# Kernel optimization log

Measured on AMD Instinct MI355X. Metric: run time of the kernel, lower is better.

Reference implementation:

```python
import jax, jax.numpy as jnp
import numpy as np
from jax import lax

RATIO = 0.5          # SAModule ratio
RADIUS = 0.15        # SAModule r
MAX_NBR = 64         # max_num_neighbors hardcoded in forward
F_IN, H1, H2, F_OUT = 64 + 3, 64, 64, 128  # local_nn MLP dims (x_j || pos_j - pos_i)


def _mlp(h, W1, b1, W2, b2, W3, b3):
    h = jax.nn.relu(h @ W1 + b1)
    h = jax.nn.relu(h @ W2 + b2)
    return jax.nn.relu(h @ W3 + b3)


def _fps_cloud(pos_c, m):
    # Farthest point sampling on one cloud [N,3]; deterministic start at index 0.
    n = pos_c.shape[0]
    def step(carry, _):
        mind, last = carry
        d = jnp.sum((pos_c - pos_c[last]) ** 2, axis=-1)
        mind = jnp.minimum(mind, d)
        nxt = jnp.argmax(mind).astype(jnp.int32)
        return (mind, nxt), last
    init = (jnp.full((n,), jnp.inf, pos_c.dtype), jnp.int32(0))
    _, sel = lax.scan(step, init, None, length=m)
    return sel  # [m] int32


def setup_inputs() -> dict:
    key = jax.random.key(0)
    ks = jax.random.split(key, 8)
    B, N, F = 8, 4096, 64
    x = jax.random.normal(ks[0], (B * N, F), jnp.float32)
    pos = jax.random.uniform(ks[1], (B * N, 3), jnp.float32)
    batch = jnp.repeat(jnp.arange(B, dtype=jnp.int64), N)
    s1 = 1.0 / np.sqrt(F_IN); s2 = 1.0 / np.sqrt(H1); s3 = 1.0 / np.sqrt(H2)
    W1 = jax.random.normal(ks[2], (F_IN, H1), jnp.float32) * s1
    b1 = jnp.zeros((H1,), jnp.float32)
    W2 = jax.random.normal(ks[3], (H1, H2), jnp.float32) * s2
    b2 = jnp.zeros((H2,), jnp.float32)
    W3 = jax.random.normal(ks[4], (H2, F_OUT), jnp.float32) * s3
    b3 = jnp.zeros((F_OUT,), jnp.float32)
    return {"x": x, "pos": pos, "batch": batch,
            "W1": W1, "b1": b1, "W2": W2, "b2": b2, "W3": W3, "b3": b3}


def reference(x, pos, batch, W1, b1, W2, b2, W3, b3):
    B = int(batch[-1]) + 1
    N = x.shape[0] // B
    M = int(N * RATIO)
    F = x.shape[1]
    xb = x.reshape(B, N, F)
    pb = pos.reshape(B, N, 3)

    # 1) fps(pos, batch, ratio)
    sel = jax.vmap(lambda p: _fps_cloud(p, M))(pb)                 # [B, M]
    q = jnp.take_along_axis(pb, sel[:, :, None], axis=1)           # [B, M, 3] centroid positions

    # 2) radius(pos, pos[idx], r, max_num_neighbors=64): keep the 64 nearest within r
    d2 = jnp.sum((q[:, :, None, :] - pb[:, None, :, :]) ** 2, -1)  # [B, M, N]
    score = jnp.where(d2 <= RADIUS ** 2, -d2, -jnp.inf)
    vals, nbr = lax.top_k(score, MAX_NBR)                          # [B, M, K]
    valid = vals > -jnp.inf                                        # centroid itself is always valid

    # 3) PointNetConv: message = net([x_j, pos_j - pos_i]); aggr = max
    xj = jax.vmap(lambda xc, i: xc[i])(xb, nbr)                    # [B, M, K, F]
    pj = jax.vmap(lambda pc, i: pc[i])(pb, nbr)                    # [B, M, K, 3]
    feat = jnp.concatenate([xj, pj - q[:, :, None, :]], axis=-1)   # [B, M, K, F+3]
    h = _mlp(feat, W1, b1, W2, b2, W3, b3)                         # [B, M, K, F_OUT]
    h = jnp.where(valid[..., None], h, -jnp.inf)
    out = jnp.max(h, axis=2)                                       # [B, M, F_OUT]

    x_out = out.reshape(B * M, -1)
    pos_out = q.reshape(B * M, 3)
    batch_out = jnp.repeat(jnp.arange(B, dtype=batch.dtype), M)
    return x_out, pos_out, batch_out
```

## Files before the change

### kernel.cpp

```cpp
#include <hip/hip_runtime.h>

typedef unsigned short u16;
typedef unsigned int u32;
typedef unsigned long long u64;

#define NB 8
#define NPTS 4096
#define MSEL 2048
#define NCENT (NB*MSEL)
#define KNBR 64
#define FEAT 64
#define FIN 67
#define HH 64
#define FOUT 128
#define CAND_CAP 192

#define KP1 96
#define SA 104
#define S2 72

typedef __attribute__((ext_vector_type(8))) short short8;
typedef __attribute__((ext_vector_type(4))) float f32x4;

__device__ __forceinline__ float bf2f(u16 u) {
    union { u32 i; float f; } v; v.i = ((u32)u) << 16; return v.f;
}
__device__ __forceinline__ u16 f2bf(float f) {
    union { float f; u32 i; } v; v.f = f;
    u32 x = v.i;
    x += 0x7fffu + ((x >> 16) & 1u);
    return (u16)(x >> 16);
}
__device__ __forceinline__ void splitbf(float a, u16& hi, u16& lo) {
    u16 h = f2bf(a);
    hi = h;
    lo = f2bf(__fsub_rn(a, bf2f(h)));
}

__device__ __forceinline__ int wave_max_i(int v) {
    int u;
    u = __builtin_amdgcn_update_dpp(v, v, 0x111, 0xf, 0xf, false); v = max(v, u);
    u = __builtin_amdgcn_update_dpp(v, v, 0x112, 0xf, 0xf, false); v = max(v, u);
    u = __builtin_amdgcn_update_dpp(v, v, 0x114, 0xf, 0xf, false); v = max(v, u);
    u = __builtin_amdgcn_update_dpp(v, v, 0x118, 0xf, 0xf, false); v = max(v, u);
    u = __builtin_amdgcn_update_dpp(v, v, 0x142, 0xf, 0xf, false); v = max(v, u);
    u = __builtin_amdgcn_update_dpp(v, v, 0x143, 0xf, 0xf, false); v = max(v, u);
    return __builtin_amdgcn_readlane(v, 63);
}
__device__ __forceinline__ int wave_min_i(int v) {
    int u;
    u = __builtin_amdgcn_update_dpp(v, v, 0x111, 0xf, 0xf, false); v = min(v, u);
    u = __builtin_amdgcn_update_dpp(v, v, 0x112, 0xf, 0xf, false); v = min(v, u);
    u = __builtin_amdgcn_update_dpp(v, v, 0x114, 0xf, 0xf, false); v = min(v, u);
    u = __builtin_amdgcn_update_dpp(v, v, 0x118, 0xf, 0xf, false); v = min(v, u);
    u = __builtin_amdgcn_update_dpp(v, v, 0x142, 0xf, 0xf, false); v = min(v, u);
    u = __builtin_amdgcn_update_dpp(v, v, 0x143, 0xf, 0xf, false); v = min(v, u);
    return __builtin_amdgcn_readlane(v, 63);
}

__global__ __launch_bounds__(256) void fps_kernel(const float* __restrict__ pos,
        int* __restrict__ sel, float* __restrict__ pos_out,
        float* __restrict__ batch_out) {
    __shared__ float px[NPTS], py[NPTS], pz[NPTS];
    __shared__ int hist[MSEL];
    __shared__ int4  sA[2][4];
    __shared__ float sZ[2][4];
    const int b = blockIdx.x, t = threadIdx.x;
    const int wid = t >> 6;
    const float* pb = pos + (long)b * NPTS * 3;

    for (int i = t; i < NPTS; i += 256) {
        px[i] = pb[i*3+0]; py[i] = pb[i*3+1]; pz[i] = pb[i*3+2];
    }
    __syncthreads();

    float rx[16], ry[16], rz[16], md[16];
    #pragma unroll
    for (int j = 0; j < 16; ++j) {
        int i = t + 256*j;
        rx[j] = px[i]; ry[j] = py[i]; rz[j] = pz[i];
        md[j] = __builtin_inff();
    }

    int cur = 0;
    float cx = px[0], cy = py[0], cz = pz[0];
    for (int s = 0; s < MSEL; ++s) {
        const int p = s & 1;
        if (t == 0) hist[s] = cur;
        float bv = -1.0f; int bi = 0;
        #pragma unroll
        for (int j = 0; j < 16; ++j) {
            float dx = __fsub_rn(rx[j], cx);
            float dy = __fsub_rn(ry[j], cy);
            float dz = __fsub_rn(rz[j], cz);
            float d  = __fadd_rn(__fadd_rn(__fmul_rn(dx,dx), __fmul_rn(dy,dy)),
                                 __fmul_rn(dz,dz));
            float m = fminf(md[j], d);
            md[j] = m;
            if (m > bv) { bv = m; bi = t + 256*j; }
        }
        const int fb = (int)__float_as_uint(bv);
        const int Mw = wave_max_i(fb);
        const int cnd = (fb == Mw) ? bi : 0x7fffffff;
        const int Iw = wave_min_i(cnd);
        if (t == (Iw & 255)) {
            int j = Iw >> 8;
            sA[p][wid] = make_int4(Mw, Iw, __float_as_int(rx[j]),
                                   __float_as_int(ry[j]));
            sZ[p][wid] = rz[j];
        }
        __syncthreads();
        int4 v0 = sA[p][0];
        int M = v0.x, I = v0.y;
        float nx = __int_as_float(v0.z), ny = __int_as_float(v0.w), nz = sZ[p][0];
        #pragma unroll
        for (int w = 1; w < 4; ++w) {
            int4 vw = sA[p][w];
            if (vw.x > M || (vw.x == M && vw.y < I)) {
                M = vw.x; I = vw.y;
                nx = __int_as_float(vw.z); ny = __int_as_float(vw.w);
                nz = sZ[p][w];
            }
        }
        cur = I; cx = nx; cy = ny; cz = nz;
    }
    __syncthreads();
    for (int g = t; g < MSEL; g += 256) {
        int i = hist[g];
        int o = b * MSEL + g;
        sel[o] = i;
        pos_out[o*3+0] = px[i]; pos_out[o*3+1] = py[i]; pos_out[o*3+2] = pz[i];
        batch_out[o] = (float)b;
    }
}

__global__ __launch_bounds__(256) void wcvt_kernel(const float* __restrict__ W1,
        const float* __restrict__ W2, const float* __restrict__ W3,
        u16* __restrict__ w1h, u16* __restrict__ w1l,
        u16* __restrict__ w2h, u16* __restrict__ w2l,
        u16* __restrict__ w3h, u16* __restrict__ w3l) {
    int t = blockIdx.x * 256 + threadIdx.x;
    if (t < 64*KP1) {
        int n = t / KP1, k = t % KP1;
        u16 h, l; splitbf((k < FIN) ? W1[(long)k*HH + n] : 0.0f, h, l);
        w1h[t] = h; w1l[t] = l;
    }
    if (t < 64*64) {
        int n = t / 64, k = t % 64;
        u16 h, l; splitbf(W2[(long)k*HH + n], h, l);
        w2h[t] = h; w2l[t] = l;
    }
    if (t < 128*64) {
        int n = t / 64, k = t % 64;
        u16 h, l; splitbf(W3[(long)k*FOUT + n], h, l);
        w3h[t] = h; w3l[t] = l;
    }
}

__global__ __launch_bounds__(256) void conv_kernel(const float* __restrict__ x,
        const float* __restrict__ pos, const int* __restrict__ sel,
        const u16* __restrict__ w1h, const u16* __restrict__ w1l,
        const u16* __restrict__ w2h, const u16* __restrict__ w2l,
        const u16* __restrict__ w3h, const u16* __restrict__ w3l,
        const float* __restrict__ b1, const float* __restrict__ b2,
        const float* __restrict__ b3, float* __restrict__ xout) {
    __shared__ __align__(16) u16 fAh[64*SA], fAl[64*SA];
    __shared__ __align__(16) u16 h1h[64*S2], h1l[64*S2];
    __shared__ float cdv[CAND_CAP];
    __shared__ int   cixv[CAND_CAP];
    __shared__ int   snbr[KNBR];
    __shared__ int   sc[2];
    const int c = blockIdx.x, t = threadIdx.x;
    const int b = c >> 11;
    const int lane = t & 63, w = t >> 6;
    const int colc = lane & 15;
    const float* pb = pos + (long)b * NPTS * 3;
    const int j0 = sel[c];
    const float qx = pb[j0*3+0], qy = pb[j0*3+1], qz = pb[j0*3+2];

    const int nw = w*16 + colc;
    const float bias1 = b1[nw];
    const float bias2 = b2[nw];
    const float bias3[2] = { b3[(2*w+0)*16 + colc], b3[(2*w+1)*16 + colc] };

    if (t == 0) { sc[0] = 0; sc[1] = 0; }
    __syncthreads();

    const float R2 = (float)(0.15 * 0.15);
    for (int it = 0; it < NPTS/256; ++it) {
        int i = t + 256*it;
        float dx = __fsub_rn(qx, pb[i*3+0]);
        float dy = __fsub_rn(qy, pb[i*3+1]);
        float dz = __fsub_rn(qz, pb[i*3+2]);
        float d2 = __fadd_rn(__fadd_rn(__fmul_rn(dx,dx), __fmul_rn(dy,dy)),
                             __fmul_rn(dz,dz));
        if (d2 <= R2) {
            int slot = atomicAdd(&sc[0], 1);
            if (slot < CAND_CAP) { cdv[slot] = d2; cixv[slot] = i; }
        }
    }
    __syncthreads();
    int C = sc[0]; if (C > CAND_CAP) C = CAND_CAP;
    int cnt;
    if (C <= KNBR) {
        for (int e = t; e < C; e += 256) snbr[e] = cixv[e];
        cnt = C;
    } else {
        for (int e = t; e < C; e += 256) {
            float de = cdv[e]; int ie = cixv[e];
            int rank = 0;
            for (int f = 0; f < C; ++f) {
                float df = cdv[f]; int jf = cixv[f];
                rank += (df < de || (df == de && jf < ie)) ? 1 : 0;
            }
            if (rank < KNBR) {
                int slot = atomicAdd(&sc[1], 1);
                snbr[slot] = ie;
            }
        }
        cnt = KNBR;
    }
    __syncthreads();

    const int kk = t >> 2, sub = t & 3;
    if (kk < cnt) {
        int j = snbr[kk];
        const float4* xr4 = (const float4*)(x + ((long)b*NPTS + j) * FEAT);
        #pragma unroll
        for (int i = 0; i < 4; ++i) {
            int ci = sub*4 + i;
            float4 v = xr4[ci];
            u16 h0,l0,h1_,l1_,h2_,l2_,h3_,l3_;
            splitbf(v.x, h0, l0); splitbf(v.y, h1_, l1_);
            splitbf(v.z, h2_, l2_); splitbf(v.w, h3_, l3_);
            int o = kk*SA + ci*4;
            fAh[o+0]=h0; fAh[o+1]=h1_; fAh[o+2]=h2_; fAh[o+3]=h3_;
            fAl[o+0]=l0; fAl[o+1]=l1_; fAl[o+2]=l2_; fAl[o+3]=l3_;
        }
        if (sub < 3) {
            float qv = (sub == 0) ? qx : ((sub == 1) ? qy : qz);
            u16 h, l; splitbf(__fsub_rn(pb[j*3+sub], qv), h, l);
            fAh[kk*SA + 64 + sub] = h; fAl[kk*SA + 64 + sub] = l;
        } else {
            fAh[kk*SA + 67] = 0; fAl[kk*SA + 67] = 0;
        }
        u32* zh = (u32*)&fAh[kk*SA + 68];
        u32* zl = (u32*)&fAl[kk*SA + 68];
        #pragma unroll
        for (int i2 = 0; i2 < 4; ++i2) { zh[sub + 4*i2] = 0; zl[sub + 4*i2] = 0; }
    }
    __syncthreads();

    const int mL = lane & 15;
    const int kq = (lane >> 4) * 8;
    const int rgrp = (lane >> 4) * 4;

    short8 B1h[3], B1l[3], B2h[2], B2l[2], B3h[2][2], B3l[2][2];
    #pragma unroll
    for (int i = 0; i < 3; ++i) {
        B1h[i] = *(const short8*)&w1h[nw*KP1 + i*32 + kq];
        B1l[i] = *(const short8*)&w1l[nw*KP1 + i*32 + kq];
    }
    #pragma unroll
    for (int i = 0; i < 2; ++i) {
        B2h[i] = *(const short8*)&w2h[nw*64 + i*32 + kq];
        B2l[i] = *(const short8*)&w2l[nw*64 + i*32 + kq];
    }

    #pragma unroll
    for (int rt = 0; rt < 4; ++rt) {
        short8 ah[3], al[3];
        #pragma unroll
        for (int i = 0; i < 3; ++i) {
            ah[i] = *(const short8*)&fAh[(rt*16 + mL)*SA + i*32 + kq];
            al[i] = *(const short8*)&fAl[(rt*16 + mL)*SA + i*32 + kq];
        }
        f32x4 acc = {bias1, bias1, bias1, bias1};
        #pragma unroll
        for (int i = 0; i < 3; ++i)
            acc = __builtin_amdgcn_mfma_f32_16x16x32_bf16(ah[i], B1h[i], acc, 0,0,0);
        #pragma unroll
        for (int i = 0; i < 3; ++i)
            acc = __builtin_amdgcn_mfma_f32_16x16x32_bf16(ah[i], B1l[i], acc, 0,0,0);
        #pragma unroll
        for (int i = 0; i < 3; ++i)
            acc = __builtin_amdgcn_mfma_f32_16x16x32_bf16(al[i], B1h[i], acc, 0,0,0);
        #pragma unroll
        for (int r = 0; r < 4; ++r) {
            u16 h, l; splitbf(fmaxf(acc[r], 0.0f), h, l);
            int mr = rt*16 + rgrp + r;
            h1h[mr*S2 + nw] = h; h1l[mr*S2 + nw] = l;
        }
    }
    #pragma unroll
    for (int j = 0; j < 2; ++j) {
        int n3 = (2*w + j)*16 + colc;
        #pragma unroll
        for (int i = 0; i < 2; ++i) {
            B3h[j][i] = *(const short8*)&w3h[n3*64 + i*32 + kq];
            B3l[j][i] = *(const short8*)&w3l[n3*64 + i*32 + kq];
        }
    }
    __syncthreads();

    #pragma unroll
    for (int rt = 0; rt < 4; ++rt) {
        short8 ah[2], al[2];
        #pragma unroll
        for (int i = 0; i < 2; ++i) {
            ah[i] = *(const short8*)&h1h[(rt*16 + mL)*S2 + i*32 + kq];
            al[i] = *(const short8*)&h1l[(rt*16 + mL)*S2 + i*32 + kq];
        }
        f32x4 acc = {bias2, bias2, bias2, bias2};
        #pragma unroll
        for (int i = 0; i < 2; ++i)
            acc = __builtin_amdgcn_mfma_f32_16x16x32_bf16(ah[i], B2h[i], acc, 0,0,0);
        #pragma unroll
        for (int i = 0; i < 2; ++i)
            acc = __builtin_amdgcn_mfma_f32_16x16x32_bf16(ah[i], B2l[i], acc, 0,0,0);
        #pragma unroll
        for (int i = 0; i < 2; ++i)
            acc = __builtin_amdgcn_mfma_f32_16x16x32_bf16(al[i], B2h[i], acc, 0,0,0);
        #pragma unroll
        for (int r = 0; r < 4; ++r) {
            u16 h, l; splitbf(fmaxf(acc[r], 0.0f), h, l);
            int mr = rt*16 + rgrp + r;
            fAh[mr*S2 + nw] = h; fAl[mr*S2 + nw] = l;
        }
    }
    __syncthreads();

    #pragma unroll
    for (int j = 0; j < 2; ++j) {
        const float bb = bias3[j];
        float v = 0.0f;
        #pragma unroll
        for (int rt = 0; rt < 4; ++rt) {
            short8 ah[2], al[2];
            #pragma unroll
            for (int i = 0; i < 2; ++i) {
                ah[i] = *(const short8*)&fAh[(rt*16 + mL)*S2 + i*32 + kq];
                al[i] = *(const short8*)&fAl[(rt*16 + mL)*S2 + i*32 + kq];
            }
            f32x4 acc = {bb, bb, bb, bb};
            #pragma unroll
            for (int i = 0; i < 2; ++i)
                acc = __builtin_amdgcn_mfma_f32_16x16x32_bf16(ah[i], B3h[j][i], acc, 0,0,0);
            #pragma unroll
            for (int i = 0; i < 2; ++i)
                acc = __builtin_amdgcn_mfma_f32_16x16x32_bf16(ah[i], B3l[j][i], acc, 0,0,0);
            #pragma unroll
            for (int i = 0; i < 2; ++i)
                acc = __builtin_amdgcn_mfma_f32_16x16x32_bf16(al[i], B3h[j][i], acc, 0,0,0);
            #pragma unroll
            for (int r = 0; r < 4; ++r) {
                int m = rt*16 + rgrp + r;
                float hv = fmaxf(acc[r], 0.0f);
                v = (m < cnt) ? fmaxf(v, hv) : v;
            }
        }
        v = fmaxf(v, __shfl_xor(v, 16, 64));
        v = fmaxf(v, __shfl_xor(v, 32, 64));
        if (lane < 16)
            xout[(long)c*FOUT + (2*w + j)*16 + lane] = v;
    }
}

extern "C" void kernel_launch(void* const* d_in, const int* in_sizes, int n_in,
                              void* d_out, int out_size, void* d_ws, size_t ws_size,
                              hipStream_t stream) {
    const float* x   = (const float*)d_in[0];
    const float* pos = (const float*)d_in[1];
    const float* W1 = (const float*)d_in[3];
    const float* b1 = (const float*)d_in[4];
    const float* W2 = (const float*)d_in[5];
    const float* b2 = (const float*)d_in[6];
    const float* W3 = (const float*)d_in[7];
    const float* b3 = (const float*)d_in[8];

    float* out       = (float*)d_out;
    float* xout      = out;
    float* pos_out   = out + (long)NCENT * FOUT;
    float* batch_out = pos_out + (long)NCENT * 3;

    int* sel = (int*)d_ws;
    u16* w1h = (u16*)((char*)d_ws + 65536);
    u16* w1l = w1h + 64*KP1;
    u16* w2h = w1l + 64*KP1;
    u16* w2l = w2h + 64*64;
    u16* w3h = w2l + 64*64;
    u16* w3l = w3h + 128*64;

    wcvt_kernel<<<32, 256, 0, stream>>>(W1, W2, W3, w1h, w1l, w2h, w2l, w3h, w3l);
    fps_kernel<<<NB, 256, 0, stream>>>(pos, sel, pos_out, batch_out);
    conv_kernel<<<NCENT, 256, 0, stream>>>(x, pos, sel, w1h, w1l, w2h, w2l,
                                           w3h, w3l, b1, b2, b3, xout);
}
```

Before: 1.950 ms.

## Widen FPS block to 512 threads with packed 64-bit DPP argmax reduction

The farthest-point-sampling kernel now runs 512 threads per cloud, so each thread holds 8 points instead of 16. The per-thread argmax becomes a tree over the 8 registers. The wave reduction packs distance and inverted index into one 64-bit key, replacing the separate max and min DPP passes. The cross-wave merge of 8 candidates also uses DPP across lanes rather than a serial loop in every thread. The aim is to shorten the 2048-step serial critical path of FPS, at the cost of more waves in the per-step barrier and more DPP traffic per step.

```diff
diff --git a/kernel.cpp b/kernel.cpp
--- a/kernel.cpp
+++ b/kernel.cpp
@@ -19,6 +19,8 @@
 #define SA 104
 #define S2 72
 
+#define FPT 512
+
 typedef __attribute__((ext_vector_type(8))) short short8;
 typedef __attribute__((ext_vector_type(4))) float f32x4;
 
@@ -37,47 +39,47 @@
     lo = f2bf(__fsub_rn(a, bf2f(h)));
 }
 
-__device__ __forceinline__ int wave_max_i(int v) {
-    int u;
-    u = __builtin_amdgcn_update_dpp(v, v, 0x111, 0xf, 0xf, false); v = max(v, u);
-    u = __builtin_amdgcn_update_dpp(v, v, 0x112, 0xf, 0xf, false); v = max(v, u);
-    u = __builtin_amdgcn_update_dpp(v, v, 0x114, 0xf, 0xf, false); v = max(v, u);
-    u = __builtin_amdgcn_update_dpp(v, v, 0x118, 0xf, 0xf, false); v = max(v, u);
-    u = __builtin_amdgcn_update_dpp(v, v, 0x142, 0xf, 0xf, false); v = max(v, u);
-    u = __builtin_amdgcn_update_dpp(v, v, 0x143, 0xf, 0xf, false); v = max(v, u);
-    return __builtin_amdgcn_readlane(v, 63);
-}
-__device__ __forceinline__ int wave_min_i(int v) {
-    int u;
-    u = __builtin_amdgcn_update_dpp(v, v, 0x111, 0xf, 0xf, false); v = min(v, u);
-    u = __builtin_amdgcn_update_dpp(v, v, 0x112, 0xf, 0xf, false); v = min(v, u);
-    u = __builtin_amdgcn_update_dpp(v, v, 0x114, 0xf, 0xf, false); v = min(v, u);
-    u = __builtin_amdgcn_update_dpp(v, v, 0x118, 0xf, 0xf, false); v = min(v, u);
-    u = __builtin_amdgcn_update_dpp(v, v, 0x142, 0xf, 0xf, false); v = min(v, u);
-    u = __builtin_amdgcn_update_dpp(v, v, 0x143, 0xf, 0xf, false); v = min(v, u);
-    return __builtin_amdgcn_readlane(v, 63);
-}
-
-__global__ __launch_bounds__(256) void fps_kernel(const float* __restrict__ pos,
+template<int CTRL>
+__device__ __forceinline__ void kstep(u32& hi, u32& lo) {
+    int h2 = __builtin_amdgcn_update_dpp((int)hi, (int)hi, CTRL, 0xf, 0xf, false);
+    int l2 = __builtin_amdgcn_update_dpp((int)lo, (int)lo, CTRL, 0xf, 0xf, false);
+    u64 a = (((u64)hi) << 32) | (u64)lo;
+    u64 c = (((u64)(u32)h2) << 32) | (u64)(u32)l2;
+    if (c > a) { hi = (u32)h2; lo = (u32)l2; }
+}
+
+template<int CTRL>
+__device__ __forceinline__ void mstep(u32& hi, u32& lo, int& x, int& y, int& z) {
+    int h2 = __builtin_amdgcn_update_dpp((int)hi, (int)hi, CTRL, 0xf, 0xf, false);
+    int l2 = __builtin_amdgcn_update_dpp((int)lo, (int)lo, CTRL, 0xf, 0xf, false);
+    int x2 = __builtin_amdgcn_update_dpp(x, x, CTRL, 0xf, 0xf, false);
+    int y2 = __builtin_amdgcn_update_dpp(y, y, CTRL, 0xf, 0xf, false);
+    int z2 = __builtin_amdgcn_update_dpp(z, z, CTRL, 0xf, 0xf, false);
+    u64 a = (((u64)hi) << 32) | (u64)lo;
+    u64 c = (((u64)(u32)h2) << 32) | (u64)(u32)l2;
+    if (c > a) { hi = (u32)h2; lo = (u32)l2; x = x2; y = y2; z = z2; }
+}
+
+__global__ __launch_bounds__(FPT) void fps_kernel(const float* __restrict__ pos,
         int* __restrict__ sel, float* __restrict__ pos_out,
         float* __restrict__ batch_out) {
     __shared__ float px[NPTS], py[NPTS], pz[NPTS];
     __shared__ int hist[MSEL];
-    __shared__ int4  sA[2][4];
-    __shared__ float sZ[2][4];
+    __shared__ int4  cA[2][8];
+    __shared__ float cZ[2][8];
     const int b = blockIdx.x, t = threadIdx.x;
-    const int wid = t >> 6;
+    const int wid = t >> 6, lane = t & 63;
     const float* pb = pos + (long)b * NPTS * 3;
 
-    for (int i = t; i < NPTS; i += 256) {
+    for (int i = t; i < NPTS; i += FPT) {
         px[i] = pb[i*3+0]; py[i] = pb[i*3+1]; pz[i] = pb[i*3+2];
     }
     __syncthreads();
 
-    float rx[16], ry[16], rz[16], md[16];
-    #pragma unroll
-    for (int j = 0; j < 16; ++j) {
-        int i = t + 256*j;
+    float rx[8], ry[8], rz[8], md[8];
+    #pragma unroll
+    for (int j = 0; j < 8; ++j) {
+        int i = t + FPT*j;
         rx[j] = px[i]; ry[j] = py[i]; rz[j] = pz[i];
         md[j] = __builtin_inff();
     }
@@ -87,45 +89,54 @@
     for (int s = 0; s < MSEL; ++s) {
         const int p = s & 1;
         if (t == 0) hist[s] = cur;
-        float bv = -1.0f; int bi = 0;
-        #pragma unroll
-        for (int j = 0; j < 16; ++j) {
+        #pragma unroll
+        for (int j = 0; j < 8; ++j) {
             float dx = __fsub_rn(rx[j], cx);
             float dy = __fsub_rn(ry[j], cy);
             float dz = __fsub_rn(rz[j], cz);
             float d  = __fadd_rn(__fadd_rn(__fmul_rn(dx,dx), __fmul_rn(dy,dy)),
                                  __fmul_rn(dz,dz));
-            float m = fminf(md[j], d);
-            md[j] = m;
-            if (m > bv) { bv = m; bi = t + 256*j; }
-        }
-        const int fb = (int)__float_as_uint(bv);
-        const int Mw = wave_max_i(fb);
-        const int cnd = (fb == Mw) ? bi : 0x7fffffff;
-        const int Iw = wave_min_i(cnd);
-        if (t == (Iw & 255)) {
-            int j = Iw >> 8;
-            sA[p][wid] = make_int4(Mw, Iw, __float_as_int(rx[j]),
-                                   __float_as_int(ry[j]));
-            sZ[p][wid] = rz[j];
+            md[j] = fminf(md[j], d);
+        }
+        float vA = md[0]; int iA = 0;
+        if (md[1] > vA) { vA = md[1]; iA = 1; }
+        float vB = md[2]; int iB = 2;
+        if (md[3] > vB) { vB = md[3]; iB = 3; }
+        if (vB > vA) { vA = vB; iA = iB; }
+        float vC = md[4]; int iC = 4;
+        if (md[5] > vC) { vC = md[5]; iC = 5; }
+        float vD = md[6]; int iD = 6;
+        if (md[7] > vD) { vD = md[7]; iD = 7; }
+        if (vD > vC) { vC = vD; iC = iD; }
+        if (vC > vA) { vA = vC; iA = iC; }
+
+        u32 hi = __float_as_uint(vA);
+        u32 lo = ~(u32)(t + (iA << 9));
+        kstep<0x111>(hi, lo); kstep<0x112>(hi, lo); kstep<0x114>(hi, lo);
+        kstep<0x118>(hi, lo); kstep<0x142>(hi, lo); kstep<0x143>(hi, lo);
+        const u32 klo = (u32)__builtin_amdgcn_readlane((int)lo, 63);
+        const u32 khi = (u32)__builtin_amdgcn_readlane((int)hi, 63);
+        const int Iw = (int)~klo;
+        if (t == (Iw & (FPT-1))) {
+            const int j = Iw >> 9;
+            cA[p][wid] = make_int4((int)khi, (int)klo,
+                                   __float_as_int(rx[j]), __float_as_int(ry[j]));
+            cZ[p][wid] = rz[j];
         }
         __syncthreads();
-        int4 v0 = sA[p][0];
-        int M = v0.x, I = v0.y;
-        float nx = __int_as_float(v0.z), ny = __int_as_float(v0.w), nz = sZ[p][0];
-        #pragma unroll
-        for (int w = 1; w < 4; ++w) {
-            int4 vw = sA[p][w];
-            if (vw.x > M || (vw.x == M && vw.y < I)) {
-                M = vw.x; I = vw.y;
-                nx = __int_as_float(vw.z); ny = __int_as_float(vw.w);
-                nz = sZ[p][w];
-            }
-        }
-        cur = I; cx = nx; cy = ny; cz = nz;
-    }
-    __syncthreads();
-    for (int g = t; g < MSEL; g += 256) {
+        int4 e = cA[p][lane & 7];
+        u32 mh = (u32)e.x, ml = (u32)e.y;
+        int mx = e.z, my = e.w, mz = __float_as_int(cZ[p][lane & 7]);
+        mstep<0x111>(mh, ml, mx, my, mz);
+        mstep<0x112>(mh, ml, mx, my, mz);
+        mstep<0x114>(mh, ml, mx, my, mz);
+        cur = (int)~(u32)__builtin_amdgcn_readlane((int)ml, 7);
+        cx = __int_as_float(__builtin_amdgcn_readlane(mx, 7));
+        cy = __int_as_float(__builtin_amdgcn_readlane(my, 7));
+        cz = __int_as_float(__builtin_amdgcn_readlane(mz, 7));
+    }
+    __syncthreads();
+    for (int g = t; g < MSEL; g += FPT) {
         int i = hist[g];
         int o = b * MSEL + g;
         sel[o] = i;
@@ -392,7 +403,7 @@
     u16* w3l = w3h + 128*64;
 
     wcvt_kernel<<<32, 256, 0, stream>>>(W1, W2, W3, w1h, w1l, w2h, w2l, w3h, w3l);
-    fps_kernel<<<NB, 256, 0, stream>>>(pos, sel, pos_out, batch_out);
+    fps_kernel<<<NB, FPT, 0, stream>>>(pos, sel, pos_out, batch_out);
     conv_kernel<<<NCENT, 256, 0, stream>>>(x, pos, sel, w1h, w1l, w2h, w2l,
                                            w3h, w3l, b1, b2, b3, xout);
 }
```

Measured after the change: 2.324 ms. 19.2% more time.

## Spatially sort FPS points into grid cells and skip distance updates via bounding-box bounds

Applied to the files above, without the earlier changes.

Before the FPS loop, each cloud's points are bucketed into an 8x8x8 grid with a counting sort, so each thread owns 16 spatially close points. Each thread keeps an axis-aligned bounding box of its points. When the box's lower-bound distance to the new centroid is already at least the thread's current best min-distance, the thread skips the distance update. When an update does change a value, the thread recomputes its local argmax with a 64-bit key reduction. This removes most per-step distance arithmetic in the serial 2048-step loop. In exchange it adds sort overhead, extra shared memory and registers, and divergent rebuild work, and it relies on a 0.99999 slack factor to stay exact.

```diff
diff --git a/kernel.cpp b/kernel.cpp
--- a/kernel.cpp
+++ b/kernel.cpp
@@ -63,6 +63,8 @@
         float* __restrict__ batch_out) {
     __shared__ float px[NPTS], py[NPTS], pz[NPTS];
     __shared__ int hist[MSEL];
+    __shared__ int sidx[NPTS];
+    __shared__ u32 cellc[512];
     __shared__ int4  sA[2][4];
     __shared__ float sZ[2][4];
     const int b = blockIdx.x, t = threadIdx.x;
@@ -72,54 +74,111 @@
     for (int i = t; i < NPTS; i += 256) {
         px[i] = pb[i*3+0]; py[i] = pb[i*3+1]; pz[i] = pb[i*3+2];
     }
+    for (int i = t; i < 512; i += 256) cellc[i] = 0;
+    __syncthreads();
+
+    for (int i = t; i < NPTS; i += 256) {
+        int qx = (int)(px[i] * 8.0f); qx = qx < 0 ? 0 : (qx > 7 ? 7 : qx);
+        int qy = (int)(py[i] * 8.0f); qy = qy < 0 ? 0 : (qy > 7 ? 7 : qy);
+        int qz = (int)(pz[i] * 8.0f); qz = qz < 0 ? 0 : (qz > 7 ? 7 : qz);
+        atomicAdd(&cellc[(qz<<6)|(qy<<3)|qx], 1u);
+    }
+    __syncthreads();
+    if (t == 0) {
+        u32 run = 0;
+        for (int c2 = 0; c2 < 512; ++c2) { u32 v = cellc[c2]; cellc[c2] = run; run += v; }
+    }
+    __syncthreads();
+    for (int i = t; i < NPTS; i += 256) {
+        int qx = (int)(px[i] * 8.0f); qx = qx < 0 ? 0 : (qx > 7 ? 7 : qx);
+        int qy = (int)(py[i] * 8.0f); qy = qy < 0 ? 0 : (qy > 7 ? 7 : qy);
+        int qz = (int)(pz[i] * 8.0f); qz = qz < 0 ? 0 : (qz > 7 ? 7 : qz);
+        u32 slot = atomicAdd(&cellc[(qz<<6)|(qy<<3)|qx], 1u);
+        sidx[slot] = i;
+    }
     __syncthreads();
 
     float rx[16], ry[16], rz[16], md[16];
+    int idx[16];
     #pragma unroll
     for (int j = 0; j < 16; ++j) {
-        int i = t + 256*j;
-        rx[j] = px[i]; ry[j] = py[i]; rz[j] = pz[i];
+        int g = sidx[t*16 + j];
+        idx[j] = g;
+        rx[j] = px[g]; ry[j] = py[g]; rz[j] = pz[g];
         md[j] = __builtin_inff();
     }
+    float lox = rx[0], hix = rx[0], loy = ry[0], hiy = ry[0], loz = rz[0], hiz = rz[0];
+    #pragma unroll
+    for (int j = 1; j < 16; ++j) {
+        lox = fminf(lox, rx[j]); hix = fmaxf(hix, rx[j]);
+        loy = fminf(loy, ry[j]); hiy = fmaxf(hiy, ry[j]);
+        loz = fminf(loz, rz[j]); hiz = fmaxf(hiz, rz[j]);
+    }
+
+    float bv, bx, by, bz; int bi;
+    auto rebuild = [&]() {
+        u64 kk[16];
+        #pragma unroll
+        for (int j = 0; j < 16; ++j)
+            kk[j] = (((u64)__float_as_uint(md[j])) << 32) | (u32)(4095 - idx[j]);
+        #pragma unroll
+        for (int st = 1; st < 16; st <<= 1) {
+            #pragma unroll
+            for (int j0 = 0; j0 < 16; j0 += 2*st) {
+                u64 a = kk[j0], c2 = kk[j0+st];
+                kk[j0] = (c2 > a) ? c2 : a;
+            }
+        }
+        bv = __uint_as_float((u32)(kk[0] >> 32));
+        bi = 4095 - (int)((u32)kk[0]);
+        #pragma unroll
+        for (int j = 0; j < 16; ++j)
+            if (idx[j] == bi) { bx = rx[j]; by = ry[j]; bz = rz[j]; }
+    };
+    rebuild();
 
     int cur = 0;
     float cx = px[0], cy = py[0], cz = pz[0];
     for (int s = 0; s < MSEL; ++s) {
         const int p = s & 1;
         if (t == 0) hist[s] = cur;
-        float bv = -1.0f; int bi = 0;
-        #pragma unroll
-        for (int j = 0; j < 16; ++j) {
-            float dx = __fsub_rn(rx[j], cx);
-            float dy = __fsub_rn(ry[j], cy);
-            float dz = __fsub_rn(rz[j], cz);
-            float d  = __fadd_rn(__fadd_rn(__fmul_rn(dx,dx), __fmul_rn(dy,dy)),
-                                 __fmul_rn(dz,dz));
-            float m = fminf(md[j], d);
-            md[j] = m;
-            if (m > bv) { bv = m; bi = t + 256*j; }
+        float ax = fmaxf(fmaxf(lox - cx, cx - hix), 0.0f);
+        float ay = fmaxf(fmaxf(loy - cy, cy - hiy), 0.0f);
+        float az = fmaxf(fmaxf(loz - cz, cz - hiz), 0.0f);
+        float lb2 = ax*ax + ay*ay + az*az;
+        if (lb2 * 0.99999f < bv) {
+            bool ch = false;
+            #pragma unroll
+            for (int j = 0; j < 16; ++j) {
+                float dx = __fsub_rn(rx[j], cx);
+                float dy = __fsub_rn(ry[j], cy);
+                float dz = __fsub_rn(rz[j], cz);
+                float d  = __fadd_rn(__fadd_rn(__fmul_rn(dx,dx), __fmul_rn(dy,dy)),
+                                     __fmul_rn(dz,dz));
+                ch |= (d < md[j]);
+                md[j] = fminf(md[j], d);
+            }
+            if (ch) rebuild();
         }
         const int fb = (int)__float_as_uint(bv);
         const int Mw = wave_max_i(fb);
         const int cnd = (fb == Mw) ? bi : 0x7fffffff;
         const int Iw = wave_min_i(cnd);
-        if (t == (Iw & 255)) {
-            int j = Iw >> 8;
-            sA[p][wid] = make_int4(Mw, Iw, __float_as_int(rx[j]),
-                                   __float_as_int(ry[j]));
-            sZ[p][wid] = rz[j];
+        if (bi == Iw) {
+            sA[p][wid] = make_int4(Mw, Iw, __float_as_int(bx), __float_as_int(by));
+            sZ[p][wid] = bz;
         }
         __syncthreads();
         int4 v0 = sA[p][0];
         int M = v0.x, I = v0.y;
         float nx = __int_as_float(v0.z), ny = __int_as_float(v0.w), nz = sZ[p][0];
         #pragma unroll
-        for (int w = 1; w < 4; ++w) {
-            int4 vw = sA[p][w];
+        for (int w2 = 1; w2 < 4; ++w2) {
+            int4 vw = sA[p][w2];
             if (vw.x > M || (vw.x == M && vw.y < I)) {
                 M = vw.x; I = vw.y;
                 nx = __int_as_float(vw.z); ny = __int_as_float(vw.w);
-                nz = sZ[p][w];
+                nz = sZ[p][w2];
             }
         }
         cur = I; cx = nx; cy = ny; cz = nz;
```

Measured after the change: 2.847 ms. 46.0% more time.

## Fuse FPS and conv into one kernel with progress-flag streaming

Applied to the files above, without the earlier changes.

Merges the farthest-point-sampling kernel and the neighbor/MLP conv kernel into a single launch. The first NB blocks run FPS and publish selected indices in chunks of 16 with a release-stored progress counter. Conv blocks spin-wait on that counter so they can start on early centroids while FPS is still running. The goal is to hide the serial FPS latency behind conv work, at the cost of relying on FPS blocks being scheduled first and of busy-waiting blocks holding CU slots.

```diff
diff --git a/kernel.cpp b/kernel.cpp
--- a/kernel.cpp
+++ b/kernel.cpp
@@ -58,88 +58,32 @@
     return __builtin_amdgcn_readlane(v, 63);
 }
 
-__global__ __launch_bounds__(256) void fps_kernel(const float* __restrict__ pos,
-        int* __restrict__ sel, float* __restrict__ pos_out,
-        float* __restrict__ batch_out) {
-    __shared__ float px[NPTS], py[NPTS], pz[NPTS];
-    __shared__ int hist[MSEL];
-    __shared__ int4  sA[2][4];
-    __shared__ float sZ[2][4];
-    const int b = blockIdx.x, t = threadIdx.x;
-    const int wid = t >> 6;
-    const float* pb = pos + (long)b * NPTS * 3;
-
-    for (int i = t; i < NPTS; i += 256) {
-        px[i] = pb[i*3+0]; py[i] = pb[i*3+1]; pz[i] = pb[i*3+2];
-    }
-    __syncthreads();
-
-    float rx[16], ry[16], rz[16], md[16];
-    #pragma unroll
-    for (int j = 0; j < 16; ++j) {
-        int i = t + 256*j;
-        rx[j] = px[i]; ry[j] = py[i]; rz[j] = pz[i];
-        md[j] = __builtin_inff();
-    }
-
-    int cur = 0;
-    float cx = px[0], cy = py[0], cz = pz[0];
-    for (int s = 0; s < MSEL; ++s) {
-        const int p = s & 1;
-        if (t == 0) hist[s] = cur;
-        float bv = -1.0f; int bi = 0;
-        #pragma unroll
-        for (int j = 0; j < 16; ++j) {
-            float dx = __fsub_rn(rx[j], cx);
-            float dy = __fsub_rn(ry[j], cy);
-            float dz = __fsub_rn(rz[j], cz);
-            float d  = __fadd_rn(__fadd_rn(__fmul_rn(dx,dx), __fmul_rn(dy,dy)),
-                                 __fmul_rn(dz,dz));
-            float m = fminf(md[j], d);
-            md[j] = m;
-            if (m > bv) { bv = m; bi = t + 256*j; }
-        }
-        const int fb = (int)__float_as_uint(bv);
-        const int Mw = wave_max_i(fb);
-        const int cnd = (fb == Mw) ? bi : 0x7fffffff;
-        const int Iw = wave_min_i(cnd);
-        if (t == (Iw & 255)) {
-            int j = Iw >> 8;
-            sA[p][wid] = make_int4(Mw, Iw, __float_as_int(rx[j]),
-                                   __float_as_int(ry[j]));
-            sZ[p][wid] = rz[j];
-        }
-        __syncthreads();
-        int4 v0 = sA[p][0];
-        int M = v0.x, I = v0.y;
-        float nx = __int_as_float(v0.z), ny = __int_as_float(v0.w), nz = sZ[p][0];
-        #pragma unroll
-        for (int w = 1; w < 4; ++w) {
-            int4 vw = sA[p][w];
-            if (vw.x > M || (vw.x == M && vw.y < I)) {
-                M = vw.x; I = vw.y;
-                nx = __int_as_float(vw.z); ny = __int_as_float(vw.w);
-                nz = sZ[p][w];
-            }
-        }
-        cur = I; cx = nx; cy = ny; cz = nz;
-    }
-    __syncthreads();
-    for (int g = t; g < MSEL; g += 256) {
-        int i = hist[g];
-        int o = b * MSEL + g;
-        sel[o] = i;
-        pos_out[o*3+0] = px[i]; pos_out[o*3+1] = py[i]; pos_out[o*3+2] = pz[i];
-        batch_out[o] = (float)b;
-    }
-}
+struct Cand { int M, I, xb, yb; };
+
+struct FpsSh {
+    float px[NPTS], py[NPTS], pz[NPTS];
+    int hist[MSEL];
+    Cand sA[2][4];
+    float sZ[2][4];
+};
+struct ConvSh {
+    u16 fAh[64*SA], fAl[64*SA];
+    u16 h1h[64*S2], h1l[64*S2];
+    float cdv[CAND_CAP];
+    int   cixv[CAND_CAP];
+    int   snbr[KNBR];
+    int   sc[2];
+};
+union __align__(16) FusedSh { FpsSh f; ConvSh c; };
 
 __global__ __launch_bounds__(256) void wcvt_kernel(const float* __restrict__ W1,
         const float* __restrict__ W2, const float* __restrict__ W3,
         u16* __restrict__ w1h, u16* __restrict__ w1l,
         u16* __restrict__ w2h, u16* __restrict__ w2l,
-        u16* __restrict__ w3h, u16* __restrict__ w3l) {
+        u16* __restrict__ w3h, u16* __restrict__ w3l,
+        u32* __restrict__ prog) {
     int t = blockIdx.x * 256 + threadIdx.x;
+    if (t < NB) prog[t] = 0;
     if (t < 64*KP1) {
         int n = t / KP1, k = t % KP1;
         u16 h, l; splitbf((k < FIN) ? W1[(long)k*HH + n] : 0.0f, h, l);
@@ -157,34 +101,129 @@
     }
 }
 
-__global__ __launch_bounds__(256) void conv_kernel(const float* __restrict__ x,
-        const float* __restrict__ pos, const int* __restrict__ sel,
+__global__ __launch_bounds__(256) void fused_kernel(const float* __restrict__ x,
+        const float* __restrict__ pos, int* __restrict__ sel,
+        u32* __restrict__ prog,
         const u16* __restrict__ w1h, const u16* __restrict__ w1l,
         const u16* __restrict__ w2h, const u16* __restrict__ w2l,
         const u16* __restrict__ w3h, const u16* __restrict__ w3l,
         const float* __restrict__ b1, const float* __restrict__ b2,
-        const float* __restrict__ b3, float* __restrict__ xout) {
-    __shared__ __align__(16) u16 fAh[64*SA], fAl[64*SA];
-    __shared__ __align__(16) u16 h1h[64*S2], h1l[64*S2];
-    __shared__ float cdv[CAND_CAP];
-    __shared__ int   cixv[CAND_CAP];
-    __shared__ int   snbr[KNBR];
-    __shared__ int   sc[2];
-    const int c = blockIdx.x, t = threadIdx.x;
+        const float* __restrict__ b3, float* __restrict__ xout,
+        float* __restrict__ pos_out, float* __restrict__ batch_out) {
+    __shared__ FusedSh S;
+    const int t = threadIdx.x;
+
+    if (blockIdx.x < NB) {
+        const int b = blockIdx.x;
+        const int wid = t >> 6;
+        const float* pb = pos + (long)b * NPTS * 3;
+
+        for (int i = t; i < NPTS; i += 256) {
+            S.f.px[i] = pb[i*3+0]; S.f.py[i] = pb[i*3+1]; S.f.pz[i] = pb[i*3+2];
+        }
+        __syncthreads();
+
+        float rx[16], ry[16], rz[16], md[16];
+        #pragma unroll
+        for (int j = 0; j < 16; ++j) {
+            int i = t + 256*j;
+            rx[j] = S.f.px[i]; ry[j] = S.f.py[i]; rz[j] = S.f.pz[i];
+            md[j] = __builtin_inff();
+        }
+
+        int cur = 0;
+        float cx = S.f.px[0], cy = S.f.py[0], cz = S.f.pz[0];
+        for (int s = 0; s < MSEL; ++s) {
+            const int p = s & 1;
+            if (t == 0) {
+                S.f.hist[s] = cur;
+                if ((s & 15) == 15) {
+                    if (s >= 16)
+                        __hip_atomic_store(&prog[b], (u32)(s - 15),
+                                           __ATOMIC_RELEASE, __HIP_MEMORY_SCOPE_AGENT);
+                    #pragma unroll
+                    for (int q = 0; q < 16; ++q) {
+                        int ss = s - 15 + q;
+                        __hip_atomic_store(&sel[(long)b*MSEL + ss], S.f.hist[ss],
+                                           __ATOMIC_RELAXED, __HIP_MEMORY_SCOPE_AGENT);
+                    }
+                }
+            }
+            float bv = -1.0f; int bi = 0;
+            #pragma unroll
+            for (int j = 0; j < 16; ++j) {
+                float dx = __fsub_rn(rx[j], cx);
+                float dy = __fsub_rn(ry[j], cy);
+                float dz = __fsub_rn(rz[j], cz);
+                float d  = __fadd_rn(__fadd_rn(__fmul_rn(dx,dx), __fmul_rn(dy,dy)),
+                                     __fmul_rn(dz,dz));
+                float m = fminf(md[j], d);
+                md[j] = m;
+                if (m > bv) { bv = m; bi = t + 256*j; }
+            }
+            const int fb = (int)__float_as_uint(bv);
+            const int Mw = wave_max_i(fb);
+            const int cnd = (fb == Mw) ? bi : 0x7fffffff;
+            const int Iw = wave_min_i(cnd);
+            if (t == (Iw & 255)) {
+                int j = Iw >> 8;
+                Cand cc; cc.M = Mw; cc.I = Iw;
+                cc.xb = __float_as_int(rx[j]); cc.yb = __float_as_int(ry[j]);
+                S.f.sA[p][wid] = cc;
+                S.f.sZ[p][wid] = rz[j];
+            }
+            __syncthreads();
+            Cand v0 = S.f.sA[p][0];
+            int M = v0.M, I = v0.I;
+            float nx = __int_as_float(v0.xb), ny = __int_as_float(v0.yb);
+            float nz = S.f.sZ[p][0];
+            #pragma unroll
+            for (int w2 = 1; w2 < 4; ++w2) {
+                Cand vw = S.f.sA[p][w2];
+                if (vw.M > M || (vw.M == M && vw.I < I)) {
+                    M = vw.M; I = vw.I;
+                    nx = __int_as_float(vw.xb); ny = __int_as_float(vw.yb);
+                    nz = S.f.sZ[p][w2];
+                }
+            }
+            cur = I; cx = nx; cy = ny; cz = nz;
+        }
+        __syncthreads();
+        if (t == 0)
+            __hip_atomic_store(&prog[b], (u32)MSEL,
+                               __ATOMIC_RELEASE, __HIP_MEMORY_SCOPE_AGENT);
+        for (int g = t; g < MSEL; g += 256) {
+            int i = S.f.hist[g];
+            int o = b * MSEL + g;
+            pos_out[o*3+0] = S.f.px[i]; pos_out[o*3+1] = S.f.py[i];
+            pos_out[o*3+2] = S.f.pz[i];
+            batch_out[o] = (float)b;
+        }
+        return;
+    }
+
+    const int c = blockIdx.x - NB;
     const int b = c >> 11;
     const int lane = t & 63, w = t >> 6;
     const int colc = lane & 15;
     const float* pb = pos + (long)b * NPTS * 3;
-    const int j0 = sel[c];
+
+    if (t == 0) {
+        S.c.sc[0] = 0; S.c.sc[1] = 0;
+        const u32 need = (u32)(c & (MSEL-1)) + 1u;
+        while (__hip_atomic_load(&prog[b], __ATOMIC_ACQUIRE,
+                                 __HIP_MEMORY_SCOPE_AGENT) < need)
+            __builtin_amdgcn_s_sleep(16);
+    }
+    __syncthreads();
+    const int j0 = (int)__hip_atomic_load(&sel[c], __ATOMIC_RELAXED,
+                                          __HIP_MEMORY_SCOPE_AGENT);
     const float qx = pb[j0*3+0], qy = pb[j0*3+1], qz = pb[j0*3+2];
 
     const int nw = w*16 + colc;
     const float bias1 = b1[nw];
     const float bias2 = b2[nw];
     const float bias3[2] = { b3[(2*w+0)*16 + colc], b3[(2*w+1)*16 + colc] };
-
-    if (t == 0) { sc[0] = 0; sc[1] = 0; }
-    __syncthreads();
 
     const float R2 = (float)(0.15 * 0.15);
     for (int it = 0; it < NPTS/256; ++it) {
@@ -195,27 +234,27 @@
         float d2 = __fadd_rn(__fadd_rn(__fmul_rn(dx,dx), __fmul_rn(dy,dy)),
                              __fmul_rn(dz,dz));
         if (d2 <= R2) {
-            int slot = atomicAdd(&sc[0], 1);
-            if (slot < CAND_CAP) { cdv[slot] = d2; cixv[slot] = i; }
-        }
-    }
-    __syncthreads();
-    int C = sc[0]; if (C > CAND_CAP) C = CAND_CAP;
+            int slot = atomicAdd(&S.c.sc[0], 1);
+            if (slot < CAND_CAP) { S.c.cdv[slot] = d2; S.c.cixv[slot] = i; }
+        }
+    }
+    __syncthreads();
+    int C = S.c.sc[0]; if (C > CAND_CAP) C = CAND_CAP;
     int cnt;
     if (C <= KNBR) {
-        for (int e = t; e < C; e += 256) snbr[e] = cixv[e];
+        for (int e = t; e < C; e += 256) S.c.snbr[e] = S.c.cixv[e];
         cnt = C;
     } else {
         for (int e = t; e < C; e += 256) {
-            float de = cdv[e]; int ie = cixv[e];
+            float de = S.c.cdv[e]; int ie = S.c.cixv[e];
             int rank = 0;
             for (int f = 0; f < C; ++f) {
-                float df = cdv[f]; int jf = cixv[f];
+                float df = S.c.cdv[f]; int jf = S.c.cixv[f];
                 rank += (df < de || (df == de && jf < ie)) ? 1 : 0;
             }
             if (rank < KNBR) {
-                int slot = atomicAdd(&sc[1], 1);
-                snbr[slot] = ie;
+                int slot = atomicAdd(&S.c.sc[1], 1);
+                S.c.snbr[slot] = ie;
             }
         }
         cnt = KNBR;
@@ -224,7 +263,7 @@
 
     const int kk = t >> 2, sub = t & 3;
     if (kk < cnt) {
-        int j = snbr[kk];
+        int j = S.c.snbr[kk];
         const float4* xr4 = (const float4*)(x + ((long)b*NPTS + j) * FEAT);
         #pragma unroll
         for (int i = 0; i < 4; ++i) {
@@ -234,18 +273,18 @@
             splitbf(v.x, h0, l0); splitbf(v.y, h1_, l1_);
             splitbf(v.z, h2_, l2_); splitbf(v.w, h3_, l3_);
             int o = kk*SA + ci*4;
-            fAh[o+0]=h0; fAh[o+1]=h1_; fAh[o+2]=h2_; fAh[o+3]=h3_;
-            fAl[o+0]=l0; fAl[o+1]=l1_; fAl[o+2]=l2_; fAl[o+3]=l3_;
+            S.c.fAh[o+0]=h0; S.c.fAh[o+1]=h1_; S.c.fAh[o+2]=h2_; S.c.fAh[o+3]=h3_;
+            S.c.fAl[o+0]=l0; S.c.fAl[o+1]=l1_; S.c.fAl[o+2]=l2_; S.c.fAl[o+3]=l3_;
         }
         if (sub < 3) {
             float qv = (sub == 0) ? qx : ((sub == 1) ? qy : qz);
             u16 h, l; splitbf(__fsub_rn(pb[j*3+sub], qv), h, l);
-            fAh[kk*SA + 64 + sub] = h; fAl[kk*SA + 64 + sub] = l;
+            S.c.fAh[kk*SA + 64 + sub] = h; S.c.fAl[kk*SA + 64 + sub] = l;
         } else {
-            fAh[kk*SA + 67] = 0; fAl[kk*SA + 67] = 0;
-        }
-        u32* zh = (u32*)&fAh[kk*SA + 68];
-        u32* zl = (u32*)&fAl[kk*SA + 68];
+            S.c.fAh[kk*SA + 67] = 0; S.c.fAl[kk*SA + 67] = 0;
+        }
+        u32* zh = (u32*)&S.c.fAh[kk*SA + 68];
+        u32* zl = (u32*)&S.c.fAl[kk*SA + 68];
         #pragma unroll
         for (int i2 = 0; i2 < 4; ++i2) { zh[sub + 4*i2] = 0; zl[sub + 4*i2] = 0; }
     }
@@ -272,8 +311,8 @@
         short8 ah[3], al[3];
         #pragma unroll
         for (int i = 0; i < 3; ++i) {
-            ah[i] = *(const short8*)&fAh[(rt*16 + mL)*SA + i*32 + kq];
-            al[i] = *(const short8*)&fAl[(rt*16 + mL)*SA + i*32 + kq];
+            ah[i] = *(const short8*)&S.c.fAh[(rt*16 + mL)*SA + i*32 + kq];
+            al[i] = *(const short8*)&S.c.fAl[(rt*16 + mL)*SA + i*32 + kq];
         }
         f32x4 acc = {bias1, bias1, bias1, bias1};
         #pragma unroll
@@ -289,7 +328,7 @@
         for (int r = 0; r < 4; ++r) {
             u16 h, l; splitbf(fmaxf(acc[r], 0.0f), h, l);
             int mr = rt*16 + rgrp + r;
-            h1h[mr*S2 + nw] = h; h1l[mr*S2 + nw] = l;
+            S.c.h1h[mr*S2 + nw] = h; S.c.h1l[mr*S2 + nw] = l;
         }
     }
     #pragma unroll
@@ -308,8 +347,8 @@
         short8 ah[2], al[2];
         #pragma unroll
         for (int i = 0; i < 2; ++i) {
-            ah[i] = *(const short8*)&h1h[(rt*16 + mL)*S2 + i*32 + kq];
-            al[i] = *(const short8*)&h1l[(rt*16 + mL)*S2 + i*32 + kq];
+            ah[i] = *(const short8*)&S.c.h1h[(rt*16 + mL)*S2 + i*32 + kq];
+            al[i] = *(const short8*)&S.c.h1l[(rt*16 + mL)*S2 + i*32 + kq];
         }
         f32x4 acc = {bias2, bias2, bias2, bias2};
         #pragma unroll
@@ -325,7 +364,7 @@
         for (int r = 0; r < 4; ++r) {
             u16 h, l; splitbf(fmaxf(acc[r], 0.0f), h, l);
             int mr = rt*16 + rgrp + r;
-            fAh[mr*S2 + nw] = h; fAl[mr*S2 + nw] = l;
+            S.c.fAh[mr*S2 + nw] = h; S.c.fAl[mr*S2 + nw] = l;
         }
     }
     __syncthreads();
@@ -339,8 +378,8 @@
             short8 ah[2], al[2];
             #pragma unroll
             for (int i = 0; i < 2; ++i) {
-                ah[i] = *(const short8*)&fAh[(rt*16 + mL)*S2 + i*32 + kq];
-                al[i] = *(const short8*)&fAl[(rt*16 + mL)*S2 + i*32 + kq];
+                ah[i] = *(const short8*)&S.c.fAh[(rt*16 + mL)*S2 + i*32 + kq];
+                al[i] = *(const short8*)&S.c.fAl[(rt*16 + mL)*S2 + i*32 + kq];
             }
             f32x4 acc = {bb, bb, bb, bb};
             #pragma unroll
@@ -390,9 +429,12 @@
     u16* w2l = w2h + 64*64;
     u16* w3h = w2l + 64*64;
     u16* w3l = w3h + 128*64;
-
-    wcvt_kernel<<<32, 256, 0, stream>>>(W1, W2, W3, w1h, w1l, w2h, w2l, w3h, w3l);
-    fps_kernel<<<NB, 256, 0, stream>>>(pos, sel, pos_out, batch_out);
-    conv_kernel<<<NCENT, 256, 0, stream>>>(x, pos, sel, w1h, w1l, w2h, w2l,
-                                           w3h, w3l, b1, b2, b3, xout);
-}
+    u32* prog = (u32*)(w3l + 128*64);
+
+    wcvt_kernel<<<32, 256, 0, stream>>>(W1, W2, W3, w1h, w1l, w2h, w2l,
+                                        w3h, w3l, prog);
+    fused_kernel<<<NB + NCENT, 256, 0, stream>>>(x, pos, sel, prog,
+                                                 w1h, w1l, w2h, w2l, w3h, w3l,
+                                                 b1, b2, b3, xout, pos_out,
+                                                 batch_out);
+}
```

Measured after the change: 2.000 ms. 1.03x slower.
